# Performance work log

Measured on AMD Instinct MI355X. Metric: run time of the kernel, lower is better.

## Reference

```python
import jax, jax.numpy as jnp
import numpy as np

B, C, H, W = 8, 256, 128, 128
WS = 8   # window size
NH = 8   # num heads
NEG = -1e9


def _rel_coords_table(ws):
    # continuous relative coords table, shape [1, 2ws-1, 2ws-1, 2]
    r = np.arange(-(ws - 1), ws, dtype=np.float32)
    t = np.stack(np.meshgrid(r, r, indexing='ij'), axis=-1)[None]
    t = t / (ws - 1) * 8.0
    t = np.sign(t) * np.log2(np.abs(t) + 1.0) / np.log2(8.0)
    return jnp.asarray(t, dtype=jnp.float32)


def _rel_pos_index(ws):
    coords = np.stack(np.meshgrid(np.arange(ws), np.arange(ws), indexing='ij'))  # [2,ws,ws]
    flat = coords.reshape(2, -1)
    rel = (flat[:, :, None] - flat[:, None, :]).transpose(1, 2, 0).astype(np.int64)  # [N,N,2]
    rel[..., 0] += ws - 1
    rel[..., 1] += ws - 1
    rel[..., 0] *= 2 * ws - 1
    return jnp.asarray(rel.sum(-1))  # [N,N]


def setup_inputs() -> dict:
    key = jax.random.key(0)
    ks = jax.random.split(key, 10)
    d8 = C // 8
    return {
        'x': jax.random.normal(ks[0], (B, C, H, W), jnp.float32),
        'y': jax.random.normal(ks[1], (B, C, H, W), jnp.float32),
        'Wq': jax.random.normal(ks[2], (d8, C), jnp.float32) * 0.02,
        'bq': jnp.zeros((d8,), jnp.float32),
        'Wk': jax.random.normal(ks[3], (d8, C), jnp.float32) * 0.02,
        'bk': jnp.zeros((d8,), jnp.float32),
        'Wv': jax.random.normal(ks[4], (C, C), jnp.float32) * 0.02,
        'bv': jnp.zeros((C,), jnp.float32),
        'gamma': jnp.full((1,), 0.5, jnp.float32),
        'qkv_w': jax.random.normal(ks[5], (3 * C, C), jnp.float32) * 0.02,
        'q_bias': jnp.zeros((C,), jnp.float32),
        'v_bias': jnp.zeros((C,), jnp.float32),
        'logit_scale': jnp.log(10.0 * jnp.ones((NH, 1, 1), jnp.float32)),
        'cpb_w1': jax.random.normal(ks[6], (512, 2), jnp.float32) * 0.02,
        'cpb_b1': jnp.zeros((512,), jnp.float32),
        'cpb_w2': jax.random.normal(ks[7], (NH, 512), jnp.float32) * 0.02,
        'proj_w': jax.random.normal(ks[8], (C, C), jnp.float32) * 0.02,
        'proj_b': jnp.zeros((C,), jnp.float32),
    }


def _criss_cross(x, y, Wq, bq, Wk, bk, Wv, bv, gamma):
    # 1x1 convs as einsum channel projections
    q = jnp.einsum('bchw,oc->bohw', x, Wq) + bq[None, :, None, None]
    k = jnp.einsum('bchw,oc->bohw', x, Wk) + bk[None, :, None, None]
    v = jnp.einsum('bchw,oc->bohw', y, Wv) + bv[None, :, None, None]
    h = x.shape[2]
    # column (H-axis) attention with -inf on diagonal; row (W-axis) attention
    diag = jnp.where(jnp.eye(h, dtype=bool), NEG, 0.0).astype(x.dtype)  # [H,H]
    eH = jnp.einsum('bchw,bcgw->bhwg', q, k) + diag[None, :, None, :]   # [B,H,W,H]
    eW = jnp.einsum('bchw,bchv->bhwv', q, k)                            # [B,H,W,W]
    att = jax.nn.softmax(jnp.concatenate([eH, eW], axis=3), axis=3)
    aH, aW = att[..., :h], att[..., h:]
    oH = jnp.einsum('bhwg,bcgw->bchw', aH, v)
    oW = jnp.einsum('bhwv,bchv->bchw', aW, v)
    return gamma[0] * (oH + oW) + x


def _window_attention(xw, qkv_w, q_bias, v_bias, logit_scale,
                      cpb_w1, cpb_b1, cpb_w2, proj_w, proj_b):
    B_, N, Cc = xw.shape
    hd = Cc // NH
    bias = jnp.concatenate([q_bias, jnp.zeros_like(v_bias), v_bias])
    qkv = (xw @ qkv_w.T + bias).reshape(B_, N, 3, NH, hd).transpose(2, 0, 3, 1, 4)
    q, k, v = qkv[0], qkv[1], qkv[2]  # [B_, NH, N, hd]
    qn = q / jnp.maximum(jnp.linalg.norm(q, axis=-1, keepdims=True), 1e-12)
    kn = k / jnp.maximum(jnp.linalg.norm(k, axis=-1, keepdims=True), 1e-12)
    scale = jnp.exp(jnp.minimum(logit_scale, jnp.log(jnp.float32(100.0))))  # [NH,1,1]
    attn = jnp.einsum('bhnd,bhmd->bhnm', qn, kn) * scale[None]
    # continuous relative position bias via inline MLP
    tbl = jax.nn.relu(_rel_coords_table(WS) @ cpb_w1.T + cpb_b1) @ cpb_w2.T  # [1,2ws-1,2ws-1,NH]
    tbl = tbl.reshape(-1, NH)
    rpb = tbl[_rel_pos_index(WS).reshape(-1)].reshape(N, N, NH).transpose(2, 0, 1)
    attn = jax.nn.softmax(attn + (16.0 * jax.nn.sigmoid(rpb))[None], axis=-1)
    out = jnp.einsum('bhnm,bhmd->bnhd', attn, v).reshape(B_, N, Cc)
    return out @ proj_w.T + proj_b


def reference(x, y, Wq, bq, Wk, bk, Wv, bv, gamma,
              qkv_w, q_bias, v_bias, logit_scale,
              cpb_w1, cpb_b1, cpb_w2, proj_w, proj_b):
    cc = _criss_cross(x, y, Wq, bq, Wk, bk, Wv, bv, gamma)   # [B,C,H,W]
    xh = cc.transpose(0, 2, 3, 1)                            # [B,H,W,C]
    win = xh.reshape(B, H // WS, WS, W // WS, WS, C)
    win = win.transpose(0, 1, 3, 2, 4, 5).reshape(-1, WS * WS, C)
    wa = _window_attention(win, qkv_w, q_bias, v_bias, logit_scale,
                           cpb_w1, cpb_b1, cpb_w2, proj_w, proj_b)
    out = wa.reshape(B, H // WS, W // WS, WS, WS, C)
    out = out.transpose(0, 1, 3, 2, 4, 5).reshape(B, H, W, C)
    return out.transpose(0, 3, 1, 2)                         # [B,C,H,W]
```

## Files before the change

kernel.cpp:

```cpp
#include <hip/hip_runtime.h>
#include <cstdio>
#include <cstddef>
#include <cstdint>

#define F_B 8
#define F_C 256
#define F_H 128
#define F_W 128
#define F_HW 16384

typedef __attribute__((ext_vector_type(8))) short short8;
typedef __attribute__((ext_vector_type(4))) short short4v;
typedef __attribute__((ext_vector_type(4))) float float4v;

__device__ __forceinline__ unsigned short f2bf(float f) {
  union {
    float f;
    uint32_t u;
  } v;
  v.f = f;
  return (unsigned short)((v.u + 0x7fffu + ((v.u >> 16) & 1u)) >> 16);
}

__device__ __forceinline__ float bf2f(unsigned short u) {
  union {
    uint32_t u;
    float f;
  } v;
  v.u = ((uint32_t)u) << 16;
  return v.f;
}

__device__ __forceinline__ void async_copy16(const unsigned short* g, unsigned short* l) {
  __builtin_amdgcn_global_load_lds((const __attribute__((address_space(1))) void*)g,
                                   (__attribute__((address_space(3))) void*)l, 16, 0, 0);
}

__global__ void build_aux2(const float* __restrict__ Wq, const float* __restrict__ Wk,
                           const float* __restrict__ bq, const float* __restrict__ bk,
                           const float* __restrict__ q_bias, const float* __restrict__ v_bias,
                           const float* __restrict__ Wv, const float* __restrict__ qkv_w,
                           const float* __restrict__ proj_w, unsigned short* __restrict__ qk_wb,
                           float* __restrict__ qk_b, float* __restrict__ qkv_b,
                           unsigned short* __restrict__ Wvb, unsigned short* __restrict__ qkv_wb,
                           unsigned short* __restrict__ proj_wb) {
  int t = blockIdx.x * 256 + threadIdx.x;
  if (t < 8192) {
    qk_wb[t] = f2bf(Wq[t]);
    qk_wb[8192 + t] = f2bf(Wk[t]);
  }
  if (t < 65536) {
    Wvb[t] = f2bf(Wv[t]);
    proj_wb[t] = f2bf(proj_w[t]);
  }
  if (t < 196608) qkv_wb[t] = f2bf(qkv_w[t]);
  if (t < 32) {
    qk_b[t] = bq[t];
    qk_b[32 + t] = bk[t];
  }
  if (t < 256) {
    qkv_b[t] = q_bias[t];
    qkv_b[256 + t] = 0.0f;
    qkv_b[512 + t] = v_bias[t];
  }
}

__device__ __forceinline__ float cpb_coord(int a) {
  float v = (float)(a - 7) * (8.0f / 7.0f);
  float lg = log2f(fabsf(v) + 1.0f) * (1.0f / 3.0f);
  return (v < 0.0f) ? -lg : lg;
}

__global__ void cpb_table(const float* __restrict__ w1, const float* __restrict__ b1,
                          const float* __restrict__ w2, float* __restrict__ tblS) {
  int e = blockIdx.x;
  int yi = e / 15, xi = e % 15;
  float ry = cpb_coord(yi), rx = cpb_coord(xi);
  __shared__ float hid[512];
  int t = threadIdx.x;
  for (int j = t; j < 512; j += 256) {
    float hv = w1[j * 2] * ry + w1[j * 2 + 1] * rx + b1[j];
    hid[j] = fmaxf(hv, 0.0f);
  }
  __syncthreads();
  if (t < 8) {
    float s = 0.0f;
    for (int j = 0; j < 512; j++) s += hid[j] * w2[t * 512 + j];
    tblS[e * 8 + t] = 16.0f / (1.0f + __expf(-s));
  }
}

__global__ void build_rpbt(const float* __restrict__ tblS, float* __restrict__ rpbt) {
  int t = blockIdx.x * 256 + threadIdx.x;
  int h = t >> 12, i = (t >> 6) & 63, j = t & 63;
  int e = ((i >> 3) - (j >> 3) + 7) * 15 + ((i & 7) - (j & 7) + 7);
  rpbt[t] = tblS[e * 8 + h];
}

__global__ void transpose_bf(const float* __restrict__ in, unsigned short* __restrict__ outb) {
  __shared__ float tile[32][33];
  int b = blockIdx.z;
  int p0 = blockIdx.x * 32;
  int c0 = blockIdx.y * 32;
  const float* src = in + (size_t)b * F_C * F_HW;
  int tx = threadIdx.x, ty = threadIdx.y;
#pragma unroll
  for (int i = 0; i < 4; i++) {
    tile[ty + i * 8][tx] = src[(size_t)(c0 + ty + i * 8) * F_HW + p0 + tx];
  }
  __syncthreads();
#pragma unroll
  for (int i = 0; i < 4; i++) {
    size_t idx = (size_t)b * F_HW * F_C + (size_t)(p0 + ty + i * 8) * F_C + c0 + tx;
    outb[idx] = f2bf(tile[tx][ty + i * 8]);
  }
}

template <int BN, int OUT>
__global__ __launch_bounds__(256) void gemm_mfma(const unsigned short* __restrict__ A,
                                                 const unsigned short* __restrict__ Wt,
                                                 const float* __restrict__ bias, void* Cmat,
                                                 int M, int N, int gx) {
  constexpr int WN = BN / 2;
  constexpr int NREP = WN / 16;
  __shared__ __align__(16) unsigned short As[128 * 32];
  __shared__ __align__(16) unsigned short Bs[BN * 32];
  int nwg = gridDim.x;
  int id = blockIdx.x;
  int cpx = nwg >> 3;
  int swz = (id & 7) * cpx + (id >> 3);
  int by = swz / gx;
  int bx = swz - by * gx;
  int m0 = by * 128;
  int n0 = bx * BN;
  int t = threadIdx.x;
  int wid = t >> 6, lane = t & 63;
  int wr = wid >> 1, wc = wid & 1;

  float4v acc[4][NREP] = {};

  for (int k0 = 0; k0 < 256; k0 += 32) {
    __syncthreads();
#pragma unroll
    for (int j = 0; j < 2; j++) {
      int r = wid * 32 + j * 16 + (lane >> 2);
      int kg = (lane & 3) ^ ((r >> 1) & 3);
      const unsigned short* gp = A + (size_t)(m0 + r) * 256 + k0 + kg * 8;
      async_copy16(gp, As + (wid * 32 + j * 16) * 32);
    }
#pragma unroll
    for (int j = 0; j < BN / 64; j++) {
      int r = wid * (BN / 4) + j * 16 + (lane >> 2);
      int kg = (lane & 3) ^ ((r >> 1) & 3);
      const unsigned short* gp = Wt + (size_t)(n0 + r) * 256 + k0 + kg * 8;
      async_copy16(gp, Bs + (wid * (BN / 4) + j * 16) * 32);
    }
    __syncthreads();
    short8 af[4];
#pragma unroll
    for (int mi = 0; mi < 4; mi++) {
      int row = wr * 64 + mi * 16 + (lane & 15);
      int kg = (lane >> 4) ^ ((row >> 1) & 3);
      af[mi] = *(const short8*)(As + row * 32 + kg * 8);
    }
    short8 bfr[NREP];
#pragma unroll
    for (int ni = 0; ni < NREP; ni++) {
      int col = wc * WN + ni * 16 + (lane & 15);
      int kg = (lane >> 4) ^ ((col >> 1) & 3);
      bfr[ni] = *(const short8*)(Bs + col * 32 + kg * 8);
    }
#pragma unroll
    for (int mi = 0; mi < 4; mi++)
#pragma unroll
      for (int ni = 0; ni < NREP; ni++)
        acc[mi][ni] =
            __builtin_amdgcn_mfma_f32_16x16x32_bf16(af[mi], bfr[ni], acc[mi][ni], 0, 0, 0);
  }
#pragma unroll
  for (int ni = 0; ni < NREP; ni++) {
    int col = n0 + wc * WN + ni * 16 + (lane & 15);
    float bn = bias[col];
#pragma unroll
    for (int mi = 0; mi < 4; mi++) {
      int row0 = m0 + wr * 64 + mi * 16 + (lane >> 4) * 4;
#pragma unroll
      for (int r = 0; r < 4; r++) {
        float v = acc[mi][ni][r] + bn;
        int row = row0 + r;
        if (OUT == 0) {
          ((float*)Cmat)[(size_t)row * N + col] = v;
        } else if (OUT == 1) {
          int bb = row >> 14, p = row & 16383;
          ((float*)Cmat)[((size_t)bb * N + col) * F_HW + p] = v;
        } else {
          ((unsigned short*)Cmat)[(size_t)row * N + col] = f2bf(v);
        }
      }
    }
  }
}

template <int MODE>
__global__ __launch_bounds__(256) void cc_logits(const float* __restrict__ qk,
                                                 unsigned short* __restrict__ e,
                                                 float* __restrict__ sums) {
  int x = blockIdx.x;
  int b = blockIdx.y;
  size_t base = (size_t)b * F_HW;
  __shared__ float kt[32][132];
  int t = threadIdx.x;
  {
    int gk = t >> 1, c0 = (t & 1) * 16;
    size_t krow = (MODE == 0) ? ((size_t)gk * F_W + x) : ((size_t)x * F_W + gk);
    const float4* src = (const float4*)(qk + (base + krow) * 64 + 32 + c0);
#pragma unroll
    for (int q4 = 0; q4 < 4; q4++) {
      float4 v = src[q4];
      kt[c0 + q4 * 4 + 0][gk] = v.x;
      kt[c0 + q4 * 4 + 1][gk] = v.y;
      kt[c0 + q4 * 4 + 2][gk] = v.z;
      kt[c0 + q4 * 4 + 3][gk] = v.w;
    }
  }
  __syncthreads();
  int i = t >> 1, g0 = (t & 1) * 64;
  size_t qrow = (MODE == 0) ? ((size_t)i * F_W + x) : ((size_t)x * F_W + i);
  const float4* qp = (const float4*)(qk + (base + qrow) * 64);
  float qreg[32];
#pragma unroll
  for (int q4 = 0; q4 < 8; q4++) {
    float4 v = qp[q4];
    qreg[q4 * 4 + 0] = v.x;
    qreg[q4 * 4 + 1] = v.y;
    qreg[q4 * 4 + 2] = v.z;
    qreg[q4 * 4 + 3] = v.w;
  }
  float acc[64];
#pragma unroll
  for (int g = 0; g < 64; g++) acc[g] = 0.0f;
  for (int c = 0; c < 32; c++) {
    float qv = qreg[c];
#pragma unroll
    for (int g = 0; g < 64; g++) acc[g] += qv * kt[c][g0 + g];
  }
  if (MODE == 0) {
    int d = i - g0;
    if (d >= 0 && d < 64) acc[d] = -1e9f;
  }
  unsigned short* ep = e + (base + qrow) * 256 + MODE * 128 + g0;
  float s = 0.0f;
#pragma unroll
  for (int g = 0; g < 64; g += 8) {
    short8 pk;
#pragma unroll
    for (int j = 0; j < 8; j++) {
      float ev = __expf(acc[g + j]);
      s += ev;
      pk[j] = (short)f2bf(ev);
    }
    *(short8*)(ep + g) = pk;
  }
  s += __shfl_xor(s, 1);
  if ((t & 1) == 0) sums[base + qrow] = s;
}

template <int MODE>
__global__ __launch_bounds__(256) void cc_pv_mfma(const unsigned short* __restrict__ eb,
                                                  const unsigned short* __restrict__ vtb,
                                                  const float* __restrict__ sumH,
                                                  const float* __restrict__ sumW,
                                                  const float* __restrict__ gamma,
                                                  const unsigned short* __restrict__ xb,
                                                  unsigned short* __restrict__ pob,
                                                  unsigned short* __restrict__ ccb) {
  int x = blockIdx.x, b = blockIdx.y;
  size_t base = (size_t)b * F_HW;
  __shared__ __align__(16) unsigned short As[128 * 128];
  __shared__ __align__(16) unsigned short Vs[256 * 64];
  int t = threadIdx.x;
  int wid = t >> 6, lane = t & 63;
  int wr = wid >> 1, wc = wid & 1;
  {
    int i = t >> 1, half = t & 1;
    size_t pix = (MODE == 0) ? ((size_t)i * F_W + x) : ((size_t)x * F_W + i);
    float rv = 1.0f / (sumH[base + pix] + sumW[base + pix]);
    const unsigned short* ep = eb + (base + pix) * 256 + MODE * 128 + half * 64;
    int g = ((i >> 3) & 7) ^ (i & 7);
#pragma unroll
    for (int s = 0; s < 8; s++) {
      short8 vin = *(const short8*)(ep + s * 8);
      short8 vo;
#pragma unroll
      for (int j = 0; j < 8; j++) vo[j] = (short)f2bf(bf2f((unsigned short)vin[j]) * rv);
      int slot = (half * 8 + s) ^ g;
      *(short8*)(As + i * 128 + slot * 8) = vo;
    }
  }
  float4v acc[4][8] = {};
#pragma unroll
  for (int kc = 0; kc < 2; kc++) {
    __syncthreads();
    {
      int ko = t >> 5, cj = t & 31;
      short8 rowv[8];
#pragma unroll
      for (int r = 0; r < 8; r++) {
        int kk = kc * 64 + ko * 8 + r;
        size_t pixk = (MODE == 0) ? ((size_t)kk * F_W + x) : ((size_t)x * F_W + kk);
        rowv[r] = *(const short8*)(vtb + (base + pixk) * 256 + cj * 8);
      }
#pragma unroll
      for (int j = 0; j < 8; j++) {
        short8 col;
#pragma unroll
        for (int r = 0; r < 8; r++) col[r] = rowv[r][j];
        int c = cj * 8 + j;
        int slot = ko ^ ((c >> 3) & 7) ^ (c & 7);
        *(short8*)(Vs + c * 64 + slot * 8) = col;
      }
    }
    __syncthreads();
#pragma unroll
    for (int ksub = 0; ksub < 2; ksub++) {
      short8 af[4];
#pragma unroll
      for (int mi = 0; mi < 4; mi++) {
        int i = wr * 64 + mi * 16 + (lane & 15);
        int slot = (kc * 8 + ksub * 4 + (lane >> 4)) ^ ((i >> 3) & 7) ^ (i & 7);
        af[mi] = *(const short8*)(As + i * 128 + slot * 8);
      }
      short8 bfv[8];
#pragma unroll
      for (int ni = 0; ni < 8; ni++) {
        int c = wc * 128 + ni * 16 + (lane & 15);
        int slot = (ksub * 4 + (lane >> 4)) ^ ((c >> 3) & 7) ^ (c & 7);
        bfv[ni] = *(const short8*)(Vs + c * 64 + slot * 8);
      }
#pragma unroll
      for (int mi = 0; mi < 4; mi++)
#pragma unroll
        for (int ni = 0; ni < 8; ni++)
          acc[mi][ni] =
              __builtin_amdgcn_mfma_f32_16x16x32_bf16(af[mi], bfv[ni], acc[mi][ni], 0, 0, 0);
    }
  }
  float gm = gamma[0];
#pragma unroll
  for (int mi = 0; mi < 4; mi++) {
#pragma unroll
    for (int ni = 0; ni < 8; ni++) {
#pragma unroll
      for (int r = 0; r < 4; r++) {
        int i = wr * 64 + mi * 16 + (lane >> 4) * 4 + r;
        int c = wc * 128 + ni * 16 + (lane & 15);
        size_t pix = (MODE == 0) ? ((size_t)i * F_W + x) : ((size_t)x * F_W + i);
        size_t idx = (base + pix) * 256 + c;
        if (MODE == 0) {
          pob[idx] = f2bf(acc[mi][ni][r]);
        } else {
          float v = gm * (bf2f(pob[idx]) + acc[mi][ni][r]) + bf2f(xb[idx]);
          ccb[idx] = f2bf(v);
        }
      }
    }
  }
}

__global__ __launch_bounds__(256) void win_attn_mfma(const unsigned short* __restrict__ qkv,
                                                     const float* __restrict__ logit_scale,
                                                     const float* __restrict__ rpbt,
                                                     unsigned short* __restrict__ out) {
  __shared__ __align__(16) unsigned short Pl[4][4096];
  __shared__ __align__(16) unsigned short Vt[4][2048];
  int win = blockIdx.x;
  int wid = threadIdx.x >> 6, lane = threadIdx.x & 63;
  int hh = blockIdx.y * 4 + wid;
  int b = win >> 8, wy = (win >> 4) & 15, wx = win & 15;
  size_t pbase = (size_t)b * F_HW + (size_t)(wy * 8) * F_W + wx * 8;
  int il = lane & 15, kg = lane >> 4;

  short8 qb[4], ka[4];
#pragma unroll
  for (int ni = 0; ni < 4; ni++) {
    int i = ni * 16 + il;
    size_t row = (pbase + (size_t)(i >> 3) * F_W + (i & 7)) * 768 + hh * 32 + kg * 8;
    short8 qv = *(const short8*)(qkv + row);
    short8 kv = *(const short8*)(qkv + row + 256);
    float qss = 0.0f, kss = 0.0f;
#pragma unroll
    for (int j = 0; j < 8; j++) {
      float qf = bf2f((unsigned short)qv[j]);
      float kf = bf2f((unsigned short)kv[j]);
      qss += qf * qf;
      kss += kf * kf;
    }
    qss += __shfl_xor(qss, 16);
    qss += __shfl_xor(qss, 32);
    kss += __shfl_xor(kss, 16);
    kss += __shfl_xor(kss, 32);
    float qinv = 1.0f / fmaxf(sqrtf(qss), 1e-12f);
    float kinv = 1.0f / fmaxf(sqrtf(kss), 1e-12f);
#pragma unroll
    for (int j = 0; j < 8; j++) {
      qb[ni][j] = (short)f2bf(bf2f((unsigned short)qv[j]) * qinv);
      ka[ni][j] = (short)f2bf(bf2f((unsigned short)kv[j]) * kinv);
    }
  }

  if (lane < 32) {
    int jb = lane >> 2, db = lane & 3;
    short8 rows[8];
#pragma unroll
    for (int r = 0; r < 8; r++) {
      rows[r] =
          *(const short8*)(qkv + (pbase + (size_t)jb * F_W + r) * 768 + hh * 32 + 512 + db * 8);
    }
#pragma unroll
    for (int c = 0; c < 8; c++) {
      int d = db * 8 + c;
      short8 col;
#pragma unroll
      for (int r = 0; r < 8; r++) col[r] = rows[r][c];
      *(short8*)(Vt[wid] + d * 64 + ((jb ^ (d & 7)) * 8)) = col;
    }
  }

  float4v sacc[4][4] = {};
#pragma unroll
  for (int mj = 0; mj < 4; mj++)
#pragma unroll
    for (int ni = 0; ni < 4; ni++)
      sacc[mj][ni] = __builtin_amdgcn_mfma_f32_16x16x32_bf16(ka[mj], qb[ni], sacc[mj][ni], 0, 0, 0);

  float scale = __expf(fminf(logit_scale[hh], 4.605170185988091f));

#pragma unroll
  for (int ni = 0; ni < 4; ni++) {
    int i = ni * 16 + il;
    const float* rp = rpbt + ((size_t)hh * 64 + i) * 64;
    float sv[16];
    float mx = -1e30f;
#pragma unroll
    for (int mj = 0; mj < 4; mj++) {
      float4 rb = *(const float4*)(rp + mj * 16 + kg * 4);
      float rbs[4] = {rb.x, rb.y, rb.z, rb.w};
#pragma unroll
      for (int r = 0; r < 4; r++) {
        float v = sacc[mj][ni][r] * scale + rbs[r];
        sv[mj * 4 + r] = v;
        mx = fmaxf(mx, v);
      }
    }
    mx = fmaxf(mx, __shfl_xor(mx, 16));
    mx = fmaxf(mx, __shfl_xor(mx, 32));
    float sm = 0.0f;
#pragma unroll
    for (int u = 0; u < 16; u++) {
      sv[u] = __expf(sv[u] - mx);
      sm += sv[u];
    }
    sm += __shfl_xor(sm, 16);
    sm += __shfl_xor(sm, 32);
    float inv = 1.0f / sm;
#pragma unroll
    for (int mj = 0; mj < 4; mj++) {
      int j0 = mj * 16 + kg * 4;
      short4v pk;
#pragma unroll
      for (int r = 0; r < 4; r++) pk[r] = (short)f2bf(sv[mj * 4 + r] * inv);
      int byteoff = i * 128 + (((j0 >> 3) ^ (i & 7)) * 16) + (j0 & 7) * 2;
      *(short4v*)((char*)Pl[wid] + byteoff) = pk;
    }
  }
  __syncthreads();

  float4v oacc[2][4] = {};
#pragma unroll
  for (int kc = 0; kc < 2; kc++) {
    short8 va[2];
#pragma unroll
    for (int md = 0; md < 2; md++) {
      int d = md * 16 + il;
      va[md] = *(const short8*)((char*)Vt[wid] + d * 128 + (((kc * 4 + kg) ^ (d & 7)) * 16));
    }
    short8 pb[4];
#pragma unroll
    for (int ni = 0; ni < 4; ni++) {
      int i = ni * 16 + il;
      pb[ni] = *(const short8*)((char*)Pl[wid] + i * 128 + (((kc * 4 + kg) ^ (i & 7)) * 16));
    }
#pragma unroll
    for (int md = 0; md < 2; md++)
#pragma unroll
      for (int ni = 0; ni < 4; ni++)
        oacc[md][ni] =
            __builtin_amdgcn_mfma_f32_16x16x32_bf16(va[md], pb[ni], oacc[md][ni], 0, 0, 0);
  }

#pragma unroll
  for (int ni = 0; ni < 4; ni++) {
    int i = ni * 16 + il;
    size_t orow = (pbase + (size_t)(i >> 3) * F_W + (i & 7)) * 256 + hh * 32;
#pragma unroll
    for (int md = 0; md < 2; md++) {
      int d0 = md * 16 + kg * 4;
      short4v pk;
#pragma unroll
      for (int r = 0; r < 4; r++) pk[r] = (short)f2bf(oacc[md][ni][r]);
      *(short4v*)(out + orow + d0) = pk;
    }
  }
}

extern "C" void kernel_launch(void* const* d_in, const int* in_sizes, int n_in,
                              void* d_out, int out_size, void* d_ws, size_t ws_size,
                              hipStream_t stream) {
  const float* x = (const float*)d_in[0];
  const float* y = (const float*)d_in[1];
  const float* Wq = (const float*)d_in[2];
  const float* bq = (const float*)d_in[3];
  const float* Wk = (const float*)d_in[4];
  const float* bk = (const float*)d_in[5];
  const float* Wv = (const float*)d_in[6];
  const float* bv = (const float*)d_in[7];
  const float* gamma = (const float*)d_in[8];
  const float* qkv_w = (const float*)d_in[9];
  const float* q_bias = (const float*)d_in[10];
  const float* v_bias = (const float*)d_in[11];
  const float* logit_scale = (const float*)d_in[12];
  const float* cpb_w1 = (const float*)d_in[13];
  const float* cpb_b1 = (const float*)d_in[14];
  const float* cpb_w2 = (const float*)d_in[15];
  const float* proj_w = (const float*)d_in[16];
  const float* proj_b = (const float*)d_in[17];

  float* ws = (float*)d_ws;
  const size_t NPX = (size_t)F_B * F_HW;
  const size_t M1 = NPX * 256;
  size_t f_xb = 0;
  size_t f_ytb = M1 / 2;
  size_t f_vtb = M1;
  size_t f_pob = M1 + M1 / 2;
  size_t f_ccb = 2 * M1;
  size_t f_qkb = 2 * M1 + M1 / 2;
  size_t f_wts = f_qkb + NPX * 64;
  size_t o_qkwb = f_wts;
  size_t o_Wvb = o_qkwb + 8192;
  size_t o_qkvwb = o_Wvb + 32768;
  size_t o_projwb = o_qkvwb + 98304;
  size_t o_qkb2 = o_projwb + 32768;
  size_t o_qkvb2 = o_qkb2 + 64;
  size_t o_tbl = o_qkvb2 + 768;
  size_t o_sumH = o_tbl + 1800;
  size_t o_sumW = o_sumH + NPX;
  size_t o_rpbt = o_sumW + NPX;
  size_t need = (o_rpbt + 32768) * sizeof(float);
  if (ws_size < need) {
    fprintf(stderr, "kernel_launch: ws too small: %zu < %zu\n", ws_size, need);
    return;
  }
  unsigned short* xb = (unsigned short*)(ws + f_xb);
  unsigned short* qkvb = (unsigned short*)(ws + f_xb);
  unsigned short* ytb = (unsigned short*)(ws + f_ytb);
  unsigned short* eb = (unsigned short*)(ws + f_ytb);
  unsigned short* vtb = (unsigned short*)(ws + f_vtb);
  unsigned short* pob = (unsigned short*)(ws + f_pob);
  unsigned short* attn_b = (unsigned short*)(ws + f_pob);
  unsigned short* ccb = (unsigned short*)(ws + f_ccb);
  float* qkb = ws + f_qkb;
  unsigned short* qk_wb = (unsigned short*)(ws + o_qkwb);
  unsigned short* Wvb = (unsigned short*)(ws + o_Wvb);
  unsigned short* qkv_wb = (unsigned short*)(ws + o_qkvwb);
  unsigned short* proj_wb = (unsigned short*)(ws + o_projwb);
  float* qk_b = ws + o_qkb2;
  float* qkv_b = ws + o_qkvb2;
  float* tblS = ws + o_tbl;
  float* sumH = ws + o_sumH;
  float* sumW = ws + o_sumW;
  float* rpbt = ws + o_rpbt;

  build_aux2<<<dim3(768), dim3(256), 0, stream>>>(Wq, Wk, bq, bk, q_bias, v_bias, Wv, qkv_w,
                                                  proj_w, qk_wb, qk_b, qkv_b, Wvb, qkv_wb,
                                                  proj_wb);
  cpb_table<<<dim3(225), dim3(256), 0, stream>>>(cpb_w1, cpb_b1, cpb_w2, tblS);
  build_rpbt<<<dim3(128), dim3(256), 0, stream>>>(tblS, rpbt);
  transpose_bf<<<dim3(512, 8, 8), dim3(32, 8), 0, stream>>>(x, xb);
  transpose_bf<<<dim3(512, 8, 8), dim3(32, 8), 0, stream>>>(y, ytb);
  gemm_mfma<64, 0><<<dim3(1024), dim3(256), 0, stream>>>(xb, qk_wb, qk_b, qkb, (int)NPX, 64,
                                                         1);
  gemm_mfma<128, 2><<<dim3(2048), dim3(256), 0, stream>>>(ytb, Wvb, bv, vtb, (int)NPX, 256, 2);
  cc_logits<0><<<dim3(128, 8), dim3(256), 0, stream>>>(qkb, eb, sumH);
  cc_logits<1><<<dim3(128, 8), dim3(256), 0, stream>>>(qkb, eb, sumW);
  cc_pv_mfma<0><<<dim3(128, 8), dim3(256), 0, stream>>>(eb, vtb, sumH, sumW, gamma, xb, pob,
                                                        ccb);
  cc_pv_mfma<1><<<dim3(128, 8), dim3(256), 0, stream>>>(eb, vtb, sumH, sumW, gamma, xb, pob,
                                                        ccb);
  gemm_mfma<128, 2><<<dim3(6144), dim3(256), 0, stream>>>(ccb, qkv_wb, qkv_b, qkvb, (int)NPX,
                                                          768, 6);
  win_attn_mfma<<<dim3(2048, 2), dim3(256), 0, stream>>>(qkvb, logit_scale, rpbt, attn_b);
  gemm_mfma<128, 1><<<dim3(2048), dim3(256), 0, stream>>>(attn_b, proj_wb, proj_b, d_out,
                                                          (int)NPX, 256, 2);
}
```

Measured before the change: 619.2 us.

## Fuse QKV projection GEMM into window attention kernel via shared-memory staging

Replaces the separate QKV GEMM and window-attention kernels with one 512-thread kernel per window. Each block loads its 64x256 window tile of the criss-cross output into LDS and computes all 768 QKV columns in six passes, streaming double-buffered weight slices. It keeps Q, K and V in LDS and then runs per-head attention, with one head per wave. This removes the global write and re-read of the large QKV intermediate. The cost is about 144KB of LDS per block, so at most one block fits per CU. Every block also re-streams the full QKV weight matrix, and the small per-block GEMM synchronises at every k step.

```diff
diff --git a/kernel.cpp b/kernel.cpp
--- a/kernel.cpp
+++ b/kernel.cpp
@@ -367,26 +367,77 @@
   }
 }
 
-__global__ __launch_bounds__(256) void win_attn_mfma(const unsigned short* __restrict__ qkv,
-                                                     const float* __restrict__ logit_scale,
-                                                     const float* __restrict__ rpbt,
-                                                     unsigned short* __restrict__ out) {
-  __shared__ __align__(16) unsigned short Pl[4][4096];
-  __shared__ __align__(16) unsigned short Vt[4][2048];
+__global__ __launch_bounds__(512, 2) void win_fused(
+    const unsigned short* __restrict__ ccb, const unsigned short* __restrict__ qkv_wb,
+    const float* __restrict__ qkv_b, const float* __restrict__ logit_scale,
+    const float* __restrict__ rpbt, unsigned short* __restrict__ out) {
+  __shared__ __align__(16) unsigned short As[64 * 256];
+  __shared__ __align__(16) unsigned short Bs[2][128 * 32];
+  __shared__ __align__(16) unsigned short QKV[3 * 64 * 256];
+  int tid = threadIdx.x;
+  int wid = tid >> 6, lane = tid & 63;
+  int il = lane & 15, kg = lane >> 4;
   int win = blockIdx.x;
-  int wid = threadIdx.x >> 6, lane = threadIdx.x & 63;
-  int hh = blockIdx.y * 4 + wid;
   int b = win >> 8, wy = (win >> 4) & 15, wx = win & 15;
   size_t pbase = (size_t)b * F_HW + (size_t)(wy * 8) * F_W + wx * 8;
-  int il = lane & 15, kg = lane >> 4;
+
+#pragma unroll
+  for (int i = 0; i < 4; i++) {
+    int n = i * 16 + (tid >> 5);
+    int slot = tid & 31;
+    size_t srow = pbase + (size_t)(n >> 3) * F_W + (n & 7);
+    async_copy16(ccb + srow * 256 + (size_t)(slot ^ (n & 7)) * 8, As + n * 256 + slot * 8);
+  }
+
+  int rB = tid >> 2, ksB = tid & 3;
+  int kgB = ksB ^ ((rB >> 1) & 3);
+  for (int nc = 0; nc < 6; nc++) {
+    int col0 = nc * 128;
+    const unsigned short* wp = qkv_wb + (size_t)(col0 + rB) * 256 + kgB * 8;
+    async_copy16(wp, Bs[0] + rB * 32 + ksB * 8);
+    __syncthreads();
+    float4v acc[4] = {};
+    int cur = 0;
+    for (int k0 = 0; k0 < 256; k0 += 32) {
+      if (k0 < 224) async_copy16(wp + k0 + 32, Bs[cur ^ 1] + rB * 32 + ksB * 8);
+      int colW = wid * 16 + il;
+      short8 bfr = *(const short8*)(Bs[cur] + colW * 32 + (kg ^ ((colW >> 1) & 3)) * 8);
+#pragma unroll
+      for (int mi = 0; mi < 4; mi++) {
+        int row = mi * 16 + il;
+        int slot = ((k0 >> 3) + kg) ^ (row & 7);
+        short8 af = *(const short8*)(As + row * 256 + slot * 8);
+        acc[mi] = __builtin_amdgcn_mfma_f32_16x16x32_bf16(af, bfr, acc[mi], 0, 0, 0);
+      }
+      __syncthreads();
+      cur ^= 1;
+    }
+    int cg = col0 + wid * 16 + il;
+    int sec = cg >> 8, cs = cg & 255;
+    float bn = qkv_b[cg];
+    unsigned short* qp = QKV + sec * 16384;
+#pragma unroll
+    for (int mi = 0; mi < 4; mi++) {
+#pragma unroll
+      for (int r = 0; r < 4; r++) {
+        int n = mi * 16 + kg * 4 + r;
+        qp[n * 256 + (((cs >> 3) ^ (n & 7)) * 8) + (cs & 7)] = f2bf(acc[mi][r] + bn);
+      }
+    }
+  }
+  __syncthreads();
+
+  int hh = wid;
+  unsigned short* Pl_w = QKV + wid * 4096;
+  unsigned short* Vt_w = As + wid * 2048;
 
   short8 qb[4], ka[4];
 #pragma unroll
   for (int ni = 0; ni < 4; ni++) {
     int i = ni * 16 + il;
-    size_t row = (pbase + (size_t)(i >> 3) * F_W + (i & 7)) * 768 + hh * 32 + kg * 8;
-    short8 qv = *(const short8*)(qkv + row);
-    short8 kv = *(const short8*)(qkv + row + 256);
+    int so = ((hh * 4 + kg) ^ (i & 7)) * 8;
+    short8 qv = *(const short8*)(QKV + i * 256 + so);
+    short8 kv = *(const short8*)(QKV + 16384 + i * 256 + so);
     float qss = 0.0f, kss = 0.0f;
 #pragma unroll
     for (int j = 0; j < 8; j++) {
@@ -413,8 +464,7 @@
     short8 rows[8];
 #pragma unroll
     for (int r = 0; r < 8; r++) {
-      rows[r] =
-          *(const short8*)(qkv + (pbase + (size_t)jb * F_W + r) * 768 + hh * 32 + 512 + db * 8);
+      rows[r] = *(const short8*)(QKV + 32768 + (jb * 8 + r) * 256 + (((hh * 4 + db) ^ r) * 8));
     }
 #pragma unroll
     for (int c = 0; c < 8; c++) {
@@ -422,7 +472,7 @@
       short8 col;
 #pragma unroll
       for (int r = 0; r < 8; r++) col[r] = rows[r][c];
-      *(short8*)(Vt[wid] + d * 64 + ((jb ^ (d & 7)) * 8)) = col;
+      *(short8*)(Vt_w + d * 64 + ((jb ^ (d & 7)) * 8)) = col;
     }
   }
 
@@ -431,9 +481,11 @@
   for (int mj = 0; mj < 4; mj++)
 #pragma unroll
     for (int ni = 0; ni < 4; ni++)
-      sacc[mj][ni] = __builtin_amdgcn_mfma_f32_16x16x32_bf16(ka[mj], qb[ni], sacc[mj][ni], 0, 0, 0);
+      sacc[mj][ni] =
+          __builtin_amdgcn_mfma_f32_16x16x32_bf16(ka[mj], qb[ni], sacc[mj][ni], 0, 0, 0);
 
   float scale = __expf(fminf(logit_scale[hh], 4.605170185988091f));
+  __syncthreads();
 
 #pragma unroll
   for (int ni = 0; ni < 4; ni++) {
@@ -470,7 +522,7 @@
 #pragma unroll
       for (int r = 0; r < 4; r++) pk[r] = (short)f2bf(sv[mj * 4 + r] * inv);
       int byteoff = i * 128 + (((j0 >> 3) ^ (i & 7)) * 16) + (j0 & 7) * 2;
-      *(short4v*)((char*)Pl[wid] + byteoff) = pk;
+      *(short4v*)((char*)Pl_w + byteoff) = pk;
     }
   }
   __syncthreads();
@@ -482,13 +534,13 @@
 #pragma unroll
     for (int md = 0; md < 2; md++) {
       int d = md * 16 + il;
-      va[md] = *(const short8*)((char*)Vt[wid] + d * 128 + (((kc * 4 + kg) ^ (d & 7)) * 16));
+      va[md] = *(const short8*)((char*)Vt_w + d * 128 + (((kc * 4 + kg) ^ (d & 7)) * 16));
     }
     short8 pb[4];
 #pragma unroll
     for (int ni = 0; ni < 4; ni++) {
       int i = ni * 16 + il;
-      pb[ni] = *(const short8*)((char*)Pl[wid] + i * 128 + (((kc * 4 + kg) ^ (i & 7)) * 16));
+      pb[ni] = *(const short8*)((char*)Pl_w + i * 128 + (((kc * 4 + kg) ^ (i & 7)) * 16));
     }
 #pragma unroll
     for (int md = 0; md < 2; md++)
@@ -561,7 +613,6 @@
     return;
   }
   unsigned short* xb = (unsigned short*)(ws + f_xb);
-  unsigned short* qkvb = (unsigned short*)(ws + f_xb);
   unsigned short* ytb = (unsigned short*)(ws + f_ytb);
   unsigned short* eb = (unsigned short*)(ws + f_ytb);
   unsigned short* vtb = (unsigned short*)(ws + f_vtb);
@@ -596,9 +647,8 @@
                                                         ccb);
   cc_pv_mfma<1><<<dim3(128, 8), dim3(256), 0, stream>>>(eb, vtb, sumH, sumW, gamma, xb, pob,
                                                         ccb);
-  gemm_mfma<128, 2><<<dim3(6144), dim3(256), 0, stream>>>(ccb, qkv_wb, qkv_b, qkvb, (int)NPX,
-                                                          768, 6);
-  win_attn_mfma<<<dim3(2048, 2), dim3(256), 0, stream>>>(qkvb, logit_scale, rpbt, attn_b);
+  win_fused<<<dim3(2048), dim3(512), 0, stream>>>(ccb, qkv_wb, qkv_b, logit_scale, rpbt,
+                                                  attn_b);
   gemm_mfma<128, 1><<<dim3(2048), dim3(256), 0, stream>>>(attn_b, proj_wb, proj_b, d_out,
                                                           (int)NPX, 256, 2);
 }
```

Result: no change. 609.8 us (-1.5%).
